# Performance work log

Hardware: AMD Instinct MI355X
Metric: run time of the kernel (lower is better)

Reference implementation:

```python
import jax, jax.numpy as jnp
import numpy as np

P = 15          # processor layers
D = 128         # node/edge feature dim (== hidden dim)
N_NODES = 10000
N_EDGES = 160000


def _mlp(x, w0, b0, w1, b1, w2, b2):
    h = jax.nn.relu(x @ w0 + b0)
    h = jax.nn.relu(h @ w1 + b1)
    return h @ w2 + b2


def setup_inputs() -> dict:
    key = jax.random.key(0)
    ks = jax.random.split(key, 20)
    inp = {
        "node_features": jax.random.normal(ks[0], (N_NODES, D), jnp.float32),
        "edge_features": jax.random.normal(ks[1], (N_EDGES, D), jnp.float32),
        "src": jax.random.randint(ks[2], (N_EDGES,), 0, N_NODES, jnp.int32),
        "dst": jax.random.randint(ks[3], (N_EDGES,), 0, N_NODES, jnp.int32),
    }
    s = 0.05
    # edge MLP: input 2*D + D = 384 -> 128 -> 128 -> 128, stacked over P layers
    inp["ew0"] = jax.random.normal(ks[4], (P, 3 * D, D), jnp.float32) * s
    inp["eb0"] = jnp.zeros((P, D), jnp.float32)
    inp["ew1"] = jax.random.normal(ks[5], (P, D, D), jnp.float32) * s
    inp["eb1"] = jnp.zeros((P, D), jnp.float32)
    inp["ew2"] = jax.random.normal(ks[6], (P, D, D), jnp.float32) * s
    inp["eb2"] = jnp.zeros((P, D), jnp.float32)
    # node MLP: input D + D = 256 -> 128 -> 128 -> 128
    inp["nw0"] = jax.random.normal(ks[7], (P, 2 * D, D), jnp.float32) * s
    inp["nb0"] = jnp.zeros((P, D), jnp.float32)
    inp["nw1"] = jax.random.normal(ks[8], (P, D, D), jnp.float32) * s
    inp["nb1"] = jnp.zeros((P, D), jnp.float32)
    inp["nw2"] = jax.random.normal(ks[9], (P, D, D), jnp.float32) * s
    inp["nb2"] = jnp.zeros((P, D), jnp.float32)
    return inp


def reference(node_features, edge_features, src, dst,
              ew0, eb0, ew1, eb1, ew2, eb2,
              nw0, nb0, nw1, nb1, nw2, nb2):
    n, e = node_features, edge_features
    for i in range(P):
        # --- edge block: gather src/dst node feats, edge MLP, residual ---
        cat_e = jnp.concatenate([n[src], n[dst], e], axis=-1)  # [E, 3D]
        e = _mlp(cat_e, ew0[i], eb0[i], ew1[i], eb1[i], ew2[i], eb2[i]) + e
        # --- node block: scatter-sum edges to dst nodes, node MLP, residual ---
        agg = jax.ops.segment_sum(e, dst, num_segments=N_NODES)  # [N, D]
        cat_n = jnp.concatenate([n, agg], axis=-1)               # [N, 2D]
        n = _mlp(cat_n, nw0[i], nb0[i], nw1[i], nb1[i], nw2[i], nb2[i]) + n
    return n
```

## Files before the change

kernel.cpp:

```cpp
#include <hip/hip_runtime.h>

#define DD 128
#define PP 15
#define NNODES 10000
#define NEDGES 160000

typedef __attribute__((ext_vector_type(8))) short bf16x8;
typedef __attribute__((ext_vector_type(4))) float f32x4;

__device__ inline ushort f2bf(float f) {
  unsigned u = __builtin_bit_cast(unsigned, f);
  u += 0x7FFFu + ((u >> 16) & 1u);
  return (ushort)(u >> 16);
}

__device__ inline float bf2f(ushort h) {
  unsigned u = ((unsigned)h) << 16;
  return __builtin_bit_cast(float, u);
}

__device__ inline f32x4 mfma16(bf16x8 a, bf16x8 b, f32x4 c) {
  return __builtin_amdgcn_mfma_f32_16x16x32_bf16(a, b, c, 0, 0, 0);
}

__global__ __launch_bounds__(256) void pack_w(const float* __restrict__ w,
                                              ushort* __restrict__ out,
                                              int K, int total) {
  int i = blockIdx.x * 256 + threadIdx.x;
  if (i >= total) return;
  int per = K * 128;
  int p = i / per, j = i % per;
  int e = j & 7;
  int lane = (j >> 3) & 63;
  int t = j >> 9;
  int nkt = K >> 5;
  int kt = t % nkt, cb = t / nkt;
  int k = kt * 32 + ((lane >> 4) << 3) + e;
  int n = (cb << 4) + (lane & 15);
  out[i] = f2bf(w[(size_t)p * per + (size_t)k * 128 + n]);
}

__global__ __launch_bounds__(256) void cvt_bf(const float* __restrict__ in,
                                              ushort* __restrict__ out, int n4) {
  int i = blockIdx.x * 256 + threadIdx.x;
  if (i >= n4) return;
  float4 v = ((const float4*)in)[i];
  ushort4 h;
  h.x = f2bf(v.x); h.y = f2bf(v.y); h.z = f2bf(v.z); h.w = f2bf(v.w);
  ((ushort4*)out)[i] = h;
}

__global__ __launch_bounds__(256) void cvt_init(const float* __restrict__ in,
                                                float* __restrict__ out_f,
                                                ushort* __restrict__ out_bf, int n4) {
  int i = blockIdx.x * 256 + threadIdx.x;
  if (i >= n4) return;
  float4 v = ((const float4*)in)[i];
  ((float4*)out_f)[i] = v;
  ushort4 h;
  h.x = f2bf(v.x); h.y = f2bf(v.y); h.z = f2bf(v.z); h.w = f2bf(v.w);
  ((ushort4*)out_bf)[i] = h;
}

__global__ __launch_bounds__(256) void hist_kernel(const int* __restrict__ dst,
                                                   int* __restrict__ cnt) {
  int i = blockIdx.x * 256 + threadIdx.x;
  if (i < NEDGES) atomicAdd(&cnt[dst[i]], 1);
}

__global__ __launch_bounds__(256) void scan_kernel(const int* __restrict__ cnt,
                                                   int* __restrict__ row_start,
                                                   int* __restrict__ cursor) {
  __shared__ int part[256];
  const int CH = (NNODES + 255) / 256;
  int t = threadIdx.x;
  int beg = t * CH, end = min(beg + CH, NNODES);
  int s = 0;
  for (int i = beg; i < end; ++i) s += cnt[i];
  part[t] = s;
  __syncthreads();
  for (int off = 1; off < 256; off <<= 1) {
    int v = (t >= off) ? part[t - off] : 0;
    __syncthreads();
    part[t] += v;
    __syncthreads();
  }
  int run = part[t] - s;
  for (int i = beg; i < end; ++i) {
    row_start[i] = run;
    cursor[i] = run;
    run += cnt[i];
  }
  if (t == 255) row_start[NNODES] = NEDGES;
}

__global__ __launch_bounds__(256) void scatter_kernel(const int* __restrict__ dst,
                                                      int* __restrict__ cursor,
                                                      int* __restrict__ eidx) {
  int i = blockIdx.x * 256 + threadIdx.x;
  if (i < NEDGES) {
    int pos = atomicAdd(&cursor[dst[i]], 1);
    eidx[pos] = i;
  }
}

__global__ __launch_bounds__(256) void agg_kernel(const ushort* __restrict__ ebf,
                                                  ushort* __restrict__ abf,
                                                  const int* __restrict__ row_start,
                                                  const int* __restrict__ eidx) {
  int wv = threadIdx.x >> 6, lane = threadIdx.x & 63;
  int node = blockIdx.x * 4 + wv;
  if (node >= NNODES) return;
  int jb = row_start[node], je = row_start[node + 1];
  float ax = 0.f, ay = 0.f, bx = 0.f, by = 0.f;
  float cx = 0.f, cy = 0.f, dx = 0.f, dy = 0.f;
  int j = jb;
  for (; j + 3 < je; j += 4) {
    int e0 = eidx[j], e1 = eidx[j + 1], e2 = eidx[j + 2], e3 = eidx[j + 3];
    uint u0 = *(const uint*)(ebf + (size_t)e0 * DD + lane * 2);
    uint u1 = *(const uint*)(ebf + (size_t)e1 * DD + lane * 2);
    uint u2 = *(const uint*)(ebf + (size_t)e2 * DD + lane * 2);
    uint u3 = *(const uint*)(ebf + (size_t)e3 * DD + lane * 2);
    ax += bf2f((ushort)u0); ay += __builtin_bit_cast(float, u0 & 0xFFFF0000u);
    bx += bf2f((ushort)u1); by += __builtin_bit_cast(float, u1 & 0xFFFF0000u);
    cx += bf2f((ushort)u2); cy += __builtin_bit_cast(float, u2 & 0xFFFF0000u);
    dx += bf2f((ushort)u3); dy += __builtin_bit_cast(float, u3 & 0xFFFF0000u);
  }
  for (; j < je; ++j) {
    int e0 = eidx[j];
    uint u0 = *(const uint*)(ebf + (size_t)e0 * DD + lane * 2);
    ax += bf2f((ushort)u0); ay += __builtin_bit_cast(float, u0 & 0xFFFF0000u);
  }
  float sx = (ax + bx) + (cx + dx);
  float sy = (ay + by) + (cy + dy);
  ushort2 h;
  h.x = f2bf(sx); h.y = f2bf(sy);
  *(ushort2*)&abf[(size_t)node * DD + lane * 2] = h;
}

__global__ __launch_bounds__(256) void edge_kernel(
    const ushort* __restrict__ nbf, ushort* __restrict__ ebf,
    const int* __restrict__ srcI, const int* __restrict__ dstI,
    const ushort* __restrict__ w0, const float* __restrict__ b0,
    const ushort* __restrict__ w1, const float* __restrict__ b1,
    const ushort* __restrict__ w2, const float* __restrict__ b2) {
  __shared__ ushort Alds[32 * 384];
  __shared__ ushort Hlds[32 * 128];
  const int tid = threadIdx.x;
  const int e0 = blockIdx.x * 32;
  const int lane = tid & 63, wv = tid >> 6;
  const int l15 = lane & 15, l4 = lane >> 4;

#pragma unroll
  for (int i = 0; i < 6; ++i) {
    int c = i * 256 + tid;
    int row = c / 48, f8 = c % 48;
    const ushort* sp;
    if (f8 < 16)       sp = nbf + (size_t)srcI[e0 + row] * DD + f8 * 8;
    else if (f8 < 32)  sp = nbf + (size_t)dstI[e0 + row] * DD + (f8 - 16) * 8;
    else               sp = ebf + (size_t)(e0 + row) * DD + (f8 - 32) * 8;
    bf16x8 v = *(const bf16x8*)sp;
    *(bf16x8*)&Alds[row * 384 + ((f8 ^ (row & 15)) * 8)] = v;
  }
  __syncthreads();

  const f32x4 z = {0.f, 0.f, 0.f, 0.f};
  const int cbA = wv * 2, cbB = wv * 2 + 1;
  f32x4 acc[2][2];

#pragma unroll
  for (int rb = 0; rb < 2; ++rb) { acc[rb][0] = z; acc[rb][1] = z; }
#pragma unroll
  for (int kt = 0; kt < 12; ++kt) {
    bf16x8 bA = *(const bf16x8*)(w0 + (size_t)((cbA * 12 + kt) * 64 + lane) * 8);
    bf16x8 bB = *(const bf16x8*)(w0 + (size_t)((cbB * 12 + kt) * 64 + lane) * 8);
#pragma unroll
    for (int rb = 0; rb < 2; ++rb) {
      int row = rb * 16 + l15;
      bf16x8 a = *(const bf16x8*)&Alds[row * 384 + (((kt * 4 + l4) ^ (row & 15)) * 8)];
      acc[rb][0] = mfma16(a, bA, acc[rb][0]);
      acc[rb][1] = mfma16(a, bB, acc[rb][1]);
    }
  }
  {
    float biasA = b0[cbA * 16 + l15], biasB = b0[cbB * 16 + l15];
#pragma unroll
    for (int cbi = 0; cbi < 2; ++cbi) {
      int col = (wv * 2 + cbi) * 16 + l15;
      float bias = cbi ? biasB : biasA;
#pragma unroll
      for (int rb = 0; rb < 2; ++rb)
#pragma unroll
        for (int r = 0; r < 4; ++r) {
          int row = rb * 16 + l4 * 4 + r;
          float v = fmaxf(acc[rb][cbi][r] + bias, 0.f);
          Hlds[row * 128 + (((col >> 3) ^ (row & 15)) * 8) + (col & 7)] = f2bf(v);
        }
    }
  }
  __syncthreads();

#pragma unroll
  for (int rb = 0; rb < 2; ++rb) { acc[rb][0] = z; acc[rb][1] = z; }
#pragma unroll
  for (int kt = 0; kt < 4; ++kt) {
    bf16x8 bA = *(const bf16x8*)(w1 + (size_t)((cbA * 4 + kt) * 64 + lane) * 8);
    bf16x8 bB = *(const bf16x8*)(w1 + (size_t)((cbB * 4 + kt) * 64 + lane) * 8);
#pragma unroll
    for (int rb = 0; rb < 2; ++rb) {
      int row = rb * 16 + l15;
      bf16x8 a = *(const bf16x8*)&Hlds[row * 128 + (((kt * 4 + l4) ^ (row & 15)) * 8)];
      acc[rb][0] = mfma16(a, bA, acc[rb][0]);
      acc[rb][1] = mfma16(a, bB, acc[rb][1]);
    }
  }
  {
    float biasA = b1[cbA * 16 + l15], biasB = b1[cbB * 16 + l15];
#pragma unroll
    for (int cbi = 0; cbi < 2; ++cbi) {
      int col = (wv * 2 + cbi) * 16 + l15;
      float bias = cbi ? biasB : biasA;
#pragma unroll
      for (int rb = 0; rb < 2; ++rb)
#pragma unroll
        for (int r = 0; r < 4; ++r) {
          int row = rb * 16 + l4 * 4 + r;
          float v = fmaxf(acc[rb][cbi][r] + bias, 0.f);
          Alds[row * 384 + (((col >> 3) ^ (row & 15)) * 8) + (col & 7)] = f2bf(v);
        }
    }
  }
  __syncthreads();

#pragma unroll
  for (int rb = 0; rb < 2; ++rb) { acc[rb][0] = z; acc[rb][1] = z; }
#pragma unroll
  for (int kt = 0; kt < 4; ++kt) {
    bf16x8 bA = *(const bf16x8*)(w2 + (size_t)((cbA * 4 + kt) * 64 + lane) * 8);
    bf16x8 bB = *(const bf16x8*)(w2 + (size_t)((cbB * 4 + kt) * 64 + lane) * 8);
#pragma unroll
    for (int rb = 0; rb < 2; ++rb) {
      int row = rb * 16 + l15;
      bf16x8 a = *(const bf16x8*)&Alds[row * 384 + (((kt * 4 + l4) ^ (row & 15)) * 8)];
      acc[rb][0] = mfma16(a, bA, acc[rb][0]);
      acc[rb][1] = mfma16(a, bB, acc[rb][1]);
    }
  }
  {
#pragma unroll
    for (int cbi = 0; cbi < 2; ++cbi) {
      int col = (wv * 2 + cbi) * 16 + l15;
      float bias = b2[col];
#pragma unroll
      for (int rb = 0; rb < 2; ++rb)
#pragma unroll
        for (int r = 0; r < 4; ++r) {
          int row = rb * 16 + l4 * 4 + r;
          float ein = bf2f(Alds[row * 384 + ((32 + ((col >> 3) ^ (row & 15))) * 8) + (col & 7)]);
          float res = ein + acc[rb][cbi][r] + bias;
          Hlds[row * 128 + (((col >> 3) ^ (row & 15)) * 8) + (col & 7)] = f2bf(res);
        }
    }
  }
  __syncthreads();
#pragma unroll
  for (int i = 0; i < 2; ++i) {
    int c = i * 256 + tid;
    int row = c >> 4, f8 = c & 15;
    bf16x8 v = *(const bf16x8*)&Hlds[row * 128 + ((f8 ^ (row & 15)) * 8)];
    *(bf16x8*)&ebf[(size_t)(e0 + row) * DD + f8 * 8] = v;
  }
}

__global__ __launch_bounds__(256) void node_kernel(
    float* __restrict__ nbuf, ushort* __restrict__ nbf,
    const ushort* __restrict__ abf,
    const ushort* __restrict__ w0, const float* __restrict__ b0,
    const ushort* __restrict__ w1, const float* __restrict__ b1,
    const ushort* __restrict__ w2, const float* __restrict__ b2) {
  __shared__ ushort Alds[32 * 256];
  __shared__ ushort Hlds[32 * 128];
  const int tid = threadIdx.x;
  const int n0 = blockIdx.x * 32;
  const int lane = tid & 63, wv = tid >> 6;
  const int l15 = lane & 15, l4 = lane >> 4;

#pragma unroll
  for (int i = 0; i < 4; ++i) {
    int c = i * 256 + tid;
    int row = c >> 5, f8 = c & 31;
    int node = n0 + row;
    bf16x8 v = {0, 0, 0, 0, 0, 0, 0, 0};
    if (node < NNODES) {
      const ushort* sp = (f8 < 16) ? nbf + (size_t)node * DD + f8 * 8
                                   : abf + (size_t)node * DD + (f8 - 16) * 8;
      v = *(const bf16x8*)sp;
    }
    *(bf16x8*)&Alds[row * 256 + ((f8 ^ (row & 15)) * 8)] = v;
  }
  __syncthreads();

  const f32x4 z = {0.f, 0.f, 0.f, 0.f};
  const int cbA = wv * 2, cbB = wv * 2 + 1;
  f32x4 acc[2][2];

#pragma unroll
  for (int rb = 0; rb < 2; ++rb) { acc[rb][0] = z; acc[rb][1] = z; }
#pragma unroll
  for (int kt = 0; kt < 8; ++kt) {
    bf16x8 bA = *(const bf16x8*)(w0 + (size_t)((cbA * 8 + kt) * 64 + lane) * 8);
    bf16x8 bB = *(const bf16x8*)(w0 + (size_t)((cbB * 8 + kt) * 64 + lane) * 8);
#pragma unroll
    for (int rb = 0; rb < 2; ++rb) {
      int row = rb * 16 + l15;
      bf16x8 a = *(const bf16x8*)&Alds[row * 256 + (((kt * 4 + l4) ^ (row & 15)) * 8)];
      acc[rb][0] = mfma16(a, bA, acc[rb][0]);
      acc[rb][1] = mfma16(a, bB, acc[rb][1]);
    }
  }
  {
    float biasA = b0[cbA * 16 + l15], biasB = b0[cbB * 16 + l15];
#pragma unroll
    for (int cbi = 0; cbi < 2; ++cbi) {
      int col = (wv * 2 + cbi) * 16 + l15;
      float bias = cbi ? biasB : biasA;
#pragma unroll
      for (int rb = 0; rb < 2; ++rb)
#pragma unroll
        for (int r = 0; r < 4; ++r) {
          int row = rb * 16 + l4 * 4 + r;
          float v = fmaxf(acc[rb][cbi][r] + bias, 0.f);
          Hlds[row * 128 + (((col >> 3) ^ (row & 15)) * 8) + (col & 7)] = f2bf(v);
        }
    }
  }
  __syncthreads();

#pragma unroll
  for (int rb = 0; rb < 2; ++rb) { acc[rb][0] = z; acc[rb][1] = z; }
#pragma unroll
  for (int kt = 0; kt < 4; ++kt) {
    bf16x8 bA = *(const bf16x8*)(w1 + (size_t)((cbA * 4 + kt) * 64 + lane) * 8);
    bf16x8 bB = *(const bf16x8*)(w1 + (size_t)((cbB * 4 + kt) * 64 + lane) * 8);
#pragma unroll
    for (int rb = 0; rb < 2; ++rb) {
      int row = rb * 16 + l15;
      bf16x8 a = *(const bf16x8*)&Hlds[row * 128 + (((kt * 4 + l4) ^ (row & 15)) * 8)];
      acc[rb][0] = mfma16(a, bA, acc[rb][0]);
      acc[rb][1] = mfma16(a, bB, acc[rb][1]);
    }
  }
  {
    float biasA = b1[cbA * 16 + l15], biasB = b1[cbB * 16 + l15];
#pragma unroll
    for (int cbi = 0; cbi < 2; ++cbi) {
      int col = (wv * 2 + cbi) * 16 + l15;
      float bias = cbi ? biasB : biasA;
#pragma unroll
      for (int rb = 0; rb < 2; ++rb)
#pragma unroll
        for (int r = 0; r < 4; ++r) {
          int row = rb * 16 + l4 * 4 + r;
          float v = fmaxf(acc[rb][cbi][r] + bias, 0.f);
          Alds[row * 256 + ((16 + ((col >> 3) ^ (row & 15))) * 8) + (col & 7)] = f2bf(v);
        }
    }
  }
  __syncthreads();

#pragma unroll
  for (int rb = 0; rb < 2; ++rb) { acc[rb][0] = z; acc[rb][1] = z; }
#pragma unroll
  for (int kt = 0; kt < 4; ++kt) {
    bf16x8 bA = *(const bf16x8*)(w2 + (size_t)((cbA * 4 + kt) * 64 + lane) * 8);
    bf16x8 bB = *(const bf16x8*)(w2 + (size_t)((cbB * 4 + kt) * 64 + lane) * 8);
#pragma unroll
    for (int rb = 0; rb < 2; ++rb) {
      int row = rb * 16 + l15;
      bf16x8 a = *(const bf16x8*)&Alds[row * 256 + ((16 + ((kt * 4 + l4) ^ (row & 15))) * 8)];
      acc[rb][0] = mfma16(a, bA, acc[rb][0]);
      acc[rb][1] = mfma16(a, bB, acc[rb][1]);
    }
  }
  {
#pragma unroll
    for (int cbi = 0; cbi < 2; ++cbi) {
      int col = (wv * 2 + cbi) * 16 + l15;
      float bias = b2[col];
#pragma unroll
      for (int rb = 0; rb < 2; ++rb)
#pragma unroll
        for (int r = 0; r < 4; ++r) {
          int row = rb * 16 + l4 * 4 + r;
          int node = n0 + row;
          if (node < NNODES) {
            size_t off = (size_t)node * DD + col;
            float res = nbuf[off] + acc[rb][cbi][r] + bias;
            nbuf[off] = res;
            nbf[off] = f2bf(res);
          }
        }
    }
  }
}

extern "C" void kernel_launch(void* const* d_in, const int* in_sizes, int n_in,
                              void* d_out, int out_size, void* d_ws, size_t ws_size,
                              hipStream_t stream) {
  const float* node_f = (const float*)d_in[0];
  const float* edge_f = (const float*)d_in[1];
  const int* srcI = (const int*)d_in[2];
  const int* dstI = (const int*)d_in[3];
  const float* ew0 = (const float*)d_in[4];
  const float* eb0 = (const float*)d_in[5];
  const float* ew1 = (const float*)d_in[6];
  const float* eb1 = (const float*)d_in[7];
  const float* ew2 = (const float*)d_in[8];
  const float* eb2 = (const float*)d_in[9];
  const float* nw0 = (const float*)d_in[10];
  const float* nb0 = (const float*)d_in[11];
  const float* nw1 = (const float*)d_in[12];
  const float* nb1 = (const float*)d_in[13];
  const float* nw2 = (const float*)d_in[14];
  const float* nb2 = (const float*)d_in[15];

  char* ws = (char*)d_ws;
  const size_t NB  = (size_t)NNODES * DD * 4;
  const size_t EBH = (size_t)NEDGES * DD * 2;
  const size_t NBH = (size_t)NNODES * DD * 2;
  ushort* ebf  = (ushort*)ws;
  float*  nbuf = (float*)(ws + EBH);
  ushort* nbf  = (ushort*)(ws + EBH + NB);
  ushort* abf  = (ushort*)(ws + EBH + NB + NBH);
  ushort* pw   = (ushort*)(ws + EBH + NB + 2 * NBH);
  ushort* pew0 = pw;
  ushort* pew1 = pew0 + 737280;
  ushort* pew2 = pew1 + 245760;
  ushort* pnw0 = pew2 + 245760;
  ushort* pnw1 = pnw0 + 491520;
  ushort* pnw2 = pnw1 + 245760;
  const size_t WBYTES = 2211840ull * 2;
  int* eidx      = (int*)(ws + EBH + NB + 2 * NBH + WBYTES);
  int* cnt       = eidx + NEDGES;
  int* row_start = cnt + NNODES;
  int* cursor    = row_start + NNODES + 1;

  {
    struct { const float* s; ushort* d; int K; } packs[6] = {
      {ew0, pew0, 384}, {ew1, pew1, 128}, {ew2, pew2, 128},
      {nw0, pnw0, 256}, {nw1, pnw1, 128}, {nw2, pnw2, 128},
    };
    for (int i = 0; i < 6; ++i) {
      int total = PP * packs[i].K * 128;
      pack_w<<<(total + 255) / 256, 256, 0, stream>>>(packs[i].s, packs[i].d,
                                                      packs[i].K, total);
    }
  }

  hipMemsetAsync(cnt, 0, NNODES * sizeof(int), stream);
  hist_kernel<<<(NEDGES + 255) / 256, 256, 0, stream>>>(dstI, cnt);
  scan_kernel<<<1, 256, 0, stream>>>(cnt, row_start, cursor);
  scatter_kernel<<<(NEDGES + 255) / 256, 256, 0, stream>>>(dstI, cursor, eidx);

  {
    int en4 = NEDGES * DD / 4, nn4 = NNODES * DD / 4;
    cvt_bf<<<(en4 + 255) / 256, 256, 0, stream>>>(edge_f, ebf, en4);
    cvt_init<<<(nn4 + 255) / 256, 256, 0, stream>>>(node_f, nbuf, nbf, nn4);
  }

  const int eblocks = NEDGES / 32;
  const int nblocks = (NNODES + 31) / 32;
  const int ablocks = (NNODES + 3) / 4;

  for (int p = 0; p < PP; ++p) {
    edge_kernel<<<eblocks, 256, 0, stream>>>(
        nbf, ebf, srcI, dstI,
        pew0 + (size_t)p * 49152, eb0 + (size_t)p * DD,
        pew1 + (size_t)p * 16384, eb1 + (size_t)p * DD,
        pew2 + (size_t)p * 16384, eb2 + (size_t)p * DD);
    agg_kernel<<<ablocks, 256, 0, stream>>>(ebf, abf, row_start, eidx);
    node_kernel<<<nblocks, 256, 0, stream>>>(
        nbuf, nbf, abf,
        pnw0 + (size_t)p * 32768, nb0 + (size_t)p * DD,
        pnw1 + (size_t)p * 16384, nb1 + (size_t)p * DD,
        pnw2 + (size_t)p * 16384, nb2 + (size_t)p * DD);
  }

  hipMemcpyAsync(d_out, nbuf, NB, hipMemcpyDeviceToDevice, stream);
}
```

Measured before the change: 1.565 ms.

## Load gathered node features directly into MFMA registers, shrink edge LDS, fuse setup kernels

The edge kernel no longer stages the src/dst node rows in a 384-wide LDS tile. Each lane now reads its gathered nbf rows straight from global memory as MFMA A-operands, and only the edge features go through a smaller LDS buffer. This cuts LDS footprint and store traffic, which may raise occupancy, at the cost of more scattered global reads per lane. The change also packs bf16 conversions with v_cvt_pk_bf16_f32, merges the six weight-pack launches and the two conversion launches into single kernels, and reuses the H buffer with an extra barrier.

```diff
diff --git a/kernel.cpp b/kernel.cpp
--- a/kernel.cpp
+++ b/kernel.cpp
@@ -19,20 +19,35 @@
   return __builtin_bit_cast(float, u);
 }
 
+__device__ inline uint cvt_pk(float lo, float hi) {
+  uint r;
+  asm("v_cvt_pk_bf16_f32 %0, %1, %2" : "=v"(r) : "v"(lo), "v"(hi));
+  return r;
+}
+
 __device__ inline f32x4 mfma16(bf16x8 a, bf16x8 b, f32x4 c) {
   return __builtin_amdgcn_mfma_f32_16x16x32_bf16(a, b, c, 0, 0, 0);
 }
 
-__global__ __launch_bounds__(256) void pack_w(const float* __restrict__ w,
-                                              ushort* __restrict__ out,
-                                              int K, int total) {
+__global__ __launch_bounds__(256) void pack_all(
+    const float* __restrict__ ew0, const float* __restrict__ ew1,
+    const float* __restrict__ ew2, const float* __restrict__ nw0,
+    const float* __restrict__ nw1, const float* __restrict__ nw2,
+    ushort* __restrict__ out) {
   int i = blockIdx.x * 256 + threadIdx.x;
-  if (i >= total) return;
+  if (i >= 2211840) return;
+  const float* w; int K; int j = i;
+  if (i < 737280)       { w = ew0; K = 384; }
+  else if (i < 983040)  { w = ew1; K = 128; j = i - 737280; }
+  else if (i < 1228800) { w = ew2; K = 128; j = i - 983040; }
+  else if (i < 1720320) { w = nw0; K = 256; j = i - 1228800; }
+  else if (i < 1966080) { w = nw1; K = 128; j = i - 1720320; }
+  else                  { w = nw2; K = 128; j = i - 1966080; }
   int per = K * 128;
-  int p = i / per, j = i % per;
-  int e = j & 7;
-  int lane = (j >> 3) & 63;
-  int t = j >> 9;
+  int p = j / per, q = j % per;
+  int e = q & 7;
+  int lane = (q >> 3) & 63;
+  int t = q >> 9;
   int nkt = K >> 5;
   int kt = t % nkt, cb = t / nkt;
   int k = kt * 32 + ((lane >> 4) << 3) + e;
@@ -40,26 +55,27 @@
   out[i] = f2bf(w[(size_t)p * per + (size_t)k * 128 + n]);
 }
 
-__global__ __launch_bounds__(256) void cvt_bf(const float* __restrict__ in,
-                                              ushort* __restrict__ out, int n4) {
+__global__ __launch_bounds__(256) void cvt_all(const float* __restrict__ ef,
+                                               const float* __restrict__ nf,
+                                               ushort* __restrict__ ebf,
+                                               float* __restrict__ nbuf,
+                                               ushort* __restrict__ nbf) {
+  const int en4 = NEDGES * DD / 4;
+  const int nn4 = NNODES * DD / 4;
   int i = blockIdx.x * 256 + threadIdx.x;
-  if (i >= n4) return;
-  float4 v = ((const float4*)in)[i];
-  ushort4 h;
-  h.x = f2bf(v.x); h.y = f2bf(v.y); h.z = f2bf(v.z); h.w = f2bf(v.w);
-  ((ushort4*)out)[i] = h;
-}
-
-__global__ __launch_bounds__(256) void cvt_init(const float* __restrict__ in,
-                                                float* __restrict__ out_f,
-                                                ushort* __restrict__ out_bf, int n4) {
-  int i = blockIdx.x * 256 + threadIdx.x;
-  if (i >= n4) return;
-  float4 v = ((const float4*)in)[i];
-  ((float4*)out_f)[i] = v;
-  ushort4 h;
-  h.x = f2bf(v.x); h.y = f2bf(v.y); h.z = f2bf(v.z); h.w = f2bf(v.w);
-  ((ushort4*)out_bf)[i] = h;
+  if (i < en4) {
+    float4 v = ((const float4*)ef)[i];
+    ushort4 h;
+    h.x = f2bf(v.x); h.y = f2bf(v.y); h.z = f2bf(v.z); h.w = f2bf(v.w);
+    ((ushort4*)ebf)[i] = h;
+  } else if (i < en4 + nn4) {
+    int k = i - en4;
+    float4 v = ((const float4*)nf)[k];
+    ((float4*)nbuf)[k] = v;
+    ushort4 h;
+    h.x = f2bf(v.x); h.y = f2bf(v.y); h.z = f2bf(v.z); h.w = f2bf(v.w);
+    ((ushort4*)nbf)[k] = h;
+  }
 }
 
 __global__ __launch_bounds__(256) void hist_kernel(const int* __restrict__ dst,
@@ -133,9 +149,7 @@
   }
   float sx = (ax + bx) + (cx + dx);
   float sy = (ay + by) + (cy + dy);
-  ushort2 h;
-  h.x = f2bf(sx); h.y = f2bf(sy);
-  *(ushort2*)&abf[(size_t)node * DD + lane * 2] = h;
+  *(uint*)&abf[(size_t)node * DD + lane * 2] = cvt_pk(sx, sy);
 }
 
 __global__ __launch_bounds__(256) void edge_kernel(
@@ -144,7 +158,7 @@
     const ushort* __restrict__ w0, const float* __restrict__ b0,
     const ushort* __restrict__ w1, const float* __restrict__ b1,
     const ushort* __restrict__ w2, const float* __restrict__ b2) {
-  __shared__ ushort Alds[32 * 384];
+  __shared__ ushort Elds[32 * 128];
   __shared__ ushort Hlds[32 * 128];
   const int tid = threadIdx.x;
   const int e0 = blockIdx.x * 32;
@@ -152,114 +166,158 @@
   const int l15 = lane & 15, l4 = lane >> 4;
 
 #pragma unroll
-  for (int i = 0; i < 6; ++i) {
+  for (int i = 0; i < 2; ++i) {
     int c = i * 256 + tid;
-    int row = c / 48, f8 = c % 48;
-    const ushort* sp;
-    if (f8 < 16)       sp = nbf + (size_t)srcI[e0 + row] * DD + f8 * 8;
-    else if (f8 < 32)  sp = nbf + (size_t)dstI[e0 + row] * DD + (f8 - 16) * 8;
-    else               sp = ebf + (size_t)(e0 + row) * DD + (f8 - 32) * 8;
-    bf16x8 v = *(const bf16x8*)sp;
-    *(bf16x8*)&Alds[row * 384 + ((f8 ^ (row & 15)) * 8)] = v;
-  }
+    int row = c >> 4, f8 = c & 15;
+    bf16x8 v = *(const bf16x8*)(ebf + (size_t)(e0 + row) * DD + f8 * 8);
+    *(bf16x8*)&Elds[row * 128 + ((f8 ^ (row & 15)) * 8)] = v;
+  }
+
+  const ushort* sp0 = nbf + (size_t)srcI[e0 + l15] * DD + l4 * 8;
+  const ushort* sp1 = nbf + (size_t)srcI[e0 + 16 + l15] * DD + l4 * 8;
+  const ushort* dp0 = nbf + (size_t)dstI[e0 + l15] * DD + l4 * 8;
+  const ushort* dp1 = nbf + (size_t)dstI[e0 + 16 + l15] * DD + l4 * 8;
   __syncthreads();
 
   const f32x4 z = {0.f, 0.f, 0.f, 0.f};
   const int cbA = wv * 2, cbB = wv * 2 + 1;
   f32x4 acc[2][2];
-
-#pragma unroll
-  for (int rb = 0; rb < 2; ++rb) { acc[rb][0] = z; acc[rb][1] = z; }
-#pragma unroll
-  for (int kt = 0; kt < 12; ++kt) {
+  acc[0][0] = z; acc[0][1] = z; acc[1][0] = z; acc[1][1] = z;
+
+#pragma unroll
+  for (int kt = 0; kt < 4; ++kt) {
     bf16x8 bA = *(const bf16x8*)(w0 + (size_t)((cbA * 12 + kt) * 64 + lane) * 8);
     bf16x8 bB = *(const bf16x8*)(w0 + (size_t)((cbB * 12 + kt) * 64 + lane) * 8);
-#pragma unroll
-    for (int rb = 0; rb < 2; ++rb) {
-      int row = rb * 16 + l15;
-      bf16x8 a = *(const bf16x8*)&Alds[row * 384 + (((kt * 4 + l4) ^ (row & 15)) * 8)];
-      acc[rb][0] = mfma16(a, bA, acc[rb][0]);
-      acc[rb][1] = mfma16(a, bB, acc[rb][1]);
-    }
-  }
+    bf16x8 a0 = *(const bf16x8*)(sp0 + kt * 32);
+    bf16x8 a1 = *(const bf16x8*)(sp1 + kt * 32);
+    acc[0][0] = mfma16(a0, bA, acc[0][0]); acc[0][1] = mfma16(a0, bB, acc[0][1]);
+    acc[1][0] = mfma16(a1, bA, acc[1][0]); acc[1][1] = mfma16(a1, bB, acc[1][1]);
+  }
+#pragma unroll
+  for (int kt = 0; kt < 4; ++kt) {
+    bf16x8 bA = *(const bf16x8*)(w0 + (size_t)((cbA * 12 + 4 + kt) * 64 + lane) * 8);
+    bf16x8 bB = *(const bf16x8*)(w0 + (size_t)((cbB * 12 + 4 + kt) * 64 + lane) * 8);
+    bf16x8 a0 = *(const bf16x8*)(dp0 + kt * 32);
+    bf16x8 a1 = *(const bf16x8*)(dp1 + kt * 32);
+    acc[0][0] = mfma16(a0, bA, acc[0][0]); acc[0][1] = mfma16(a0, bB, acc[0][1]);
+    acc[1][0] = mfma16(a1, bA, acc[1][0]); acc[1][1] = mfma16(a1, bB, acc[1][1]);
+  }
+#pragma unroll
+  for (int kt = 0; kt < 4; ++kt) {
+    bf16x8 bA = *(const bf16x8*)(w0 + (size_t)((cbA * 12 + 8 + kt) * 64 + lane) * 8);
+    bf16x8 bB = *(const bf16x8*)(w0 + (size_t)((cbB * 12 + 8 + kt) * 64 + lane) * 8);
+    int sl = ((kt * 4 + l4) ^ l15) * 8;
+    bf16x8 a0 = *(const bf16x8*)&Elds[l15 * 128 + sl];
+    bf16x8 a1 = *(const bf16x8*)&Elds[(16 + l15) * 128 + sl];
+    acc[0][0] = mfma16(a0, bA, acc[0][0]); acc[0][1] = mfma16(a0, bB, acc[0][1]);
+    acc[1][0] = mfma16(a1, bA, acc[1][0]); acc[1][1] = mfma16(a1, bB, acc[1][1]);
+  }
+
   {
     float biasA = b0[cbA * 16 + l15], biasB = b0[cbB * 16 + l15];
 #pragma unroll
     for (int cbi = 0; cbi < 2; ++cbi) {
       int col = (wv * 2 + cbi) * 16 + l15;
       float bias = cbi ? biasB : biasA;
-#pragma unroll
-      for (int rb = 0; rb < 2; ++rb)
-#pragma unroll
-        for (int r = 0; r < 4; ++r) {
-          int row = rb * 16 + l4 * 4 + r;
-          float v = fmaxf(acc[rb][cbi][r] + bias, 0.f);
-          Hlds[row * 128 + (((col >> 3) ^ (row & 15)) * 8) + (col & 7)] = f2bf(v);
-        }
-    }
-  }
-  __syncthreads();
-
-#pragma unroll
-  for (int rb = 0; rb < 2; ++rb) { acc[rb][0] = z; acc[rb][1] = z; }
+      int cs = col >> 3, c7 = col & 7;
+#pragma unroll
+      for (int rb = 0; rb < 2; ++rb) {
+        float v0 = fmaxf(acc[rb][cbi][0] + bias, 0.f);
+        float v1 = fmaxf(acc[rb][cbi][1] + bias, 0.f);
+        float v2 = fmaxf(acc[rb][cbi][2] + bias, 0.f);
+        float v3 = fmaxf(acc[rb][cbi][3] + bias, 0.f);
+        uint p01 = cvt_pk(v0, v1), p23 = cvt_pk(v2, v3);
+        int r0 = rb * 16 + l4 * 4;
+        Hlds[(r0 + 0) * 128 + ((cs ^ ((r0 + 0) & 15)) * 8) + c7] = (ushort)p01;
+        Hlds[(r0 + 1) * 128 + ((cs ^ ((r0 + 1) & 15)) * 8) + c7] = (ushort)(p01 >> 16);
+        Hlds[(r0 + 2) * 128 + ((cs ^ ((r0 + 2) & 15)) * 8) + c7] = (ushort)p23;
+        Hlds[(r0 + 3) * 128 + ((cs ^ ((r0 + 3) & 15)) * 8) + c7] = (ushort)(p23 >> 16);
+      }
+    }
+  }
+  __syncthreads();
+
+  acc[0][0] = z; acc[0][1] = z; acc[1][0] = z; acc[1][1] = z;
 #pragma unroll
   for (int kt = 0; kt < 4; ++kt) {
     bf16x8 bA = *(const bf16x8*)(w1 + (size_t)((cbA * 4 + kt) * 64 + lane) * 8);
     bf16x8 bB = *(const bf16x8*)(w1 + (size_t)((cbB * 4 + kt) * 64 + lane) * 8);
-#pragma unroll
-    for (int rb = 0; rb < 2; ++rb) {
-      int row = rb * 16 + l15;
-      bf16x8 a = *(const bf16x8*)&Hlds[row * 128 + (((kt * 4 + l4) ^ (row & 15)) * 8)];
-      acc[rb][0] = mfma16(a, bA, acc[rb][0]);
-      acc[rb][1] = mfma16(a, bB, acc[rb][1]);
-    }
-  }
+    int sl = ((kt * 4 + l4) ^ l15) * 8;
+    bf16x8 a0 = *(const bf16x8*)&Hlds[l15 * 128 + sl];
+    bf16x8 a1 = *(const bf16x8*)&Hlds[(16 + l15) * 128 + sl];
+    acc[0][0] = mfma16(a0, bA, acc[0][0]); acc[0][1] = mfma16(a0, bB, acc[0][1]);
+    acc[1][0] = mfma16(a1, bA, acc[1][0]); acc[1][1] = mfma16(a1, bB, acc[1][1]);
+  }
+  uint h2p[2][2][2];
   {
     float biasA = b1[cbA * 16 + l15], biasB = b1[cbB * 16 + l15];
 #pragma unroll
     for (int cbi = 0; cbi < 2; ++cbi) {
+      float bias = cbi ? biasB : biasA;
+#pragma unroll
+      for (int rb = 0; rb < 2; ++rb) {
+        float v0 = fmaxf(acc[rb][cbi][0] + bias, 0.f);
+        float v1 = fmaxf(acc[rb][cbi][1] + bias, 0.f);
+        float v2 = fmaxf(acc[rb][cbi][2] + bias, 0.f);
+        float v3 = fmaxf(acc[rb][cbi][3] + bias, 0.f);
+        h2p[rb][cbi][0] = cvt_pk(v0, v1);
+        h2p[rb][cbi][1] = cvt_pk(v2, v3);
+      }
+    }
+  }
+  __syncthreads();
+  {
+#pragma unroll
+    for (int cbi = 0; cbi < 2; ++cbi) {
       int col = (wv * 2 + cbi) * 16 + l15;
-      float bias = cbi ? biasB : biasA;
-#pragma unroll
-      for (int rb = 0; rb < 2; ++rb)
-#pragma unroll
-        for (int r = 0; r < 4; ++r) {
-          int row = rb * 16 + l4 * 4 + r;
-          float v = fmaxf(acc[rb][cbi][r] + bias, 0.f);
-          Alds[row * 384 + (((col >> 3) ^ (row & 15)) * 8) + (col & 7)] = f2bf(v);
-        }
-    }
-  }
-  __syncthreads();
-
-#pragma unroll
-  for (int rb = 0; rb < 2; ++rb) { acc[rb][0] = z; acc[rb][1] = z; }
+      int cs = col >> 3, c7 = col & 7;
+#pragma unroll
+      for (int rb = 0; rb < 2; ++rb) {
+        uint p01 = h2p[rb][cbi][0], p23 = h2p[rb][cbi][1];
+        int r0 = rb * 16 + l4 * 4;
+        Hlds[(r0 + 0) * 128 + ((cs ^ ((r0 + 0) & 15)) * 8) + c7] = (ushort)p01;
+        Hlds[(r0 + 1) * 128 + ((cs ^ ((r0 + 1) & 15)) * 8) + c7] = (ushort)(p01 >> 16);
+        Hlds[(r0 + 2) * 128 + ((cs ^ ((r0 + 2) & 15)) * 8) + c7] = (ushort)p23;
+        Hlds[(r0 + 3) * 128 + ((cs ^ ((r0 + 3) & 15)) * 8) + c7] = (ushort)(p23 >> 16);
+      }
+    }
+  }
+  __syncthreads();
+
+  acc[0][0] = z; acc[0][1] = z; acc[1][0] = z; acc[1][1] = z;
 #pragma unroll
   for (int kt = 0; kt < 4; ++kt) {
     bf16x8 bA = *(const bf16x8*)(w2 + (size_t)((cbA * 4 + kt) * 64 + lane) * 8);
     bf16x8 bB = *(const bf16x8*)(w2 + (size_t)((cbB * 4 + kt) * 64 + lane) * 8);
-#pragma unroll
-    for (int rb = 0; rb < 2; ++rb) {
-      int row = rb * 16 + l15;
-      bf16x8 a = *(const bf16x8*)&Alds[row * 384 + (((kt * 4 + l4) ^ (row & 15)) * 8)];
-      acc[rb][0] = mfma16(a, bA, acc[rb][0]);
-      acc[rb][1] = mfma16(a, bB, acc[rb][1]);
-    }
+    int sl = ((kt * 4 + l4) ^ l15) * 8;
+    bf16x8 a0 = *(const bf16x8*)&Hlds[l15 * 128 + sl];
+    bf16x8 a1 = *(const bf16x8*)&Hlds[(16 + l15) * 128 + sl];
+    acc[0][0] = mfma16(a0, bA, acc[0][0]); acc[0][1] = mfma16(a0, bB, acc[0][1]);
+    acc[1][0] = mfma16(a1, bA, acc[1][0]); acc[1][1] = mfma16(a1, bB, acc[1][1]);
   }
   {
 #pragma unroll
     for (int cbi = 0; cbi < 2; ++cbi) {
       int col = (wv * 2 + cbi) * 16 + l15;
       float bias = b2[col];
-#pragma unroll
-      for (int rb = 0; rb < 2; ++rb)
-#pragma unroll
-        for (int r = 0; r < 4; ++r) {
-          int row = rb * 16 + l4 * 4 + r;
-          float ein = bf2f(Alds[row * 384 + ((32 + ((col >> 3) ^ (row & 15))) * 8) + (col & 7)]);
-          float res = ein + acc[rb][cbi][r] + bias;
-          Hlds[row * 128 + (((col >> 3) ^ (row & 15)) * 8) + (col & 7)] = f2bf(res);
-        }
+      int cs = col >> 3, c7 = col & 7;
+#pragma unroll
+      for (int rb = 0; rb < 2; ++rb) {
+        int r0 = rb * 16 + l4 * 4;
+        int i0 = (r0 + 0) * 128 + ((cs ^ ((r0 + 0) & 15)) * 8) + c7;
+        int i1 = (r0 + 1) * 128 + ((cs ^ ((r0 + 1) & 15)) * 8) + c7;
+        int i2 = (r0 + 2) * 128 + ((cs ^ ((r0 + 2) & 15)) * 8) + c7;
+        int i3 = (r0 + 3) * 128 + ((cs ^ ((r0 + 3) & 15)) * 8) + c7;
+        float v0 = bf2f(Elds[i0]) + acc[rb][cbi][0] + bias;
+        float v1 = bf2f(Elds[i1]) + acc[rb][cbi][1] + bias;
+        float v2 = bf2f(Elds[i2]) + acc[rb][cbi][2] + bias;
+        float v3 = bf2f(Elds[i3]) + acc[rb][cbi][3] + bias;
+        uint p01 = cvt_pk(v0, v1), p23 = cvt_pk(v2, v3);
+        Elds[i0] = (ushort)p01;
+        Elds[i1] = (ushort)(p01 >> 16);
+        Elds[i2] = (ushort)p23;
+        Elds[i3] = (ushort)(p23 >> 16);
+      }
     }
   }
   __syncthreads();
@@ -267,7 +325,7 @@
   for (int i = 0; i < 2; ++i) {
     int c = i * 256 + tid;
     int row = c >> 4, f8 = c & 15;
-    bf16x8 v = *(const bf16x8*)&Hlds[row * 128 + ((f8 ^ (row & 15)) * 8)];
+    bf16x8 v = *(const bf16x8*)&Elds[row * 128 + ((f8 ^ (row & 15)) * 8)];
     *(bf16x8*)&ebf[(size_t)(e0 + row) * DD + f8 * 8] = v;
   }
 }
@@ -304,19 +362,16 @@
   const int cbA = wv * 2, cbB = wv * 2 + 1;
   f32x4 acc[2][2];
 
-#pragma unroll
-  for (int rb = 0; rb < 2; ++rb) { acc[rb][0] = z; acc[rb][1] = z; }
+  acc[0][0] = z; acc[0][1] = z; acc[1][0] = z; acc[1][1] = z;
 #pragma unroll
   for (int kt = 0; kt < 8; ++kt) {
     bf16x8 bA = *(const bf16x8*)(w0 + (size_t)((cbA * 8 + kt) * 64 + lane) * 8);
     bf16x8 bB = *(const bf16x8*)(w0 + (size_t)((cbB * 8 + kt) * 64 + lane) * 8);
-#pragma unroll
-    for (int rb = 0; rb < 2; ++rb) {
-      int row = rb * 16 + l15;
-      bf16x8 a = *(const bf16x8*)&Alds[row * 256 + (((kt * 4 + l4) ^ (row & 15)) * 8)];
-      acc[rb][0] = mfma16(a, bA, acc[rb][0]);
-      acc[rb][1] = mfma16(a, bB, acc[rb][1]);
-    }
+    int sl = ((kt * 4 + l4) ^ l15) * 8;
+    bf16x8 a0 = *(const bf16x8*)&Alds[l15 * 256 + sl];
+    bf16x8 a1 = *(const bf16x8*)&Alds[(16 + l15) * 256 + sl];
+    acc[0][0] = mfma16(a0, bA, acc[0][0]); acc[0][1] = mfma16(a0, bB, acc[0][1]);
+    acc[1][0] = mfma16(a1, bA, acc[1][0]); acc[1][1] = mfma16(a1, bB, acc[1][1]);
   }
   {
     float biasA = b0[cbA * 16 + l15], biasB = b0[cbB * 16 + l15];
@@ -324,31 +379,34 @@
     for (int cbi = 0; cbi < 2; ++cbi) {
       int col = (wv * 2 + cbi) * 16 + l15;
       float bias = cbi ? biasB : biasA;
-#pragma unroll
-      for (int rb = 0; rb < 2; ++rb)
-#pragma unroll
-        for (int r = 0; r < 4; ++r) {
-          int row = rb * 16 + l4 * 4 + r;
-          float v = fmaxf(acc[rb][cbi][r] + bias, 0.f);
-          Hlds[row * 128 + (((col >> 3) ^ (row & 15)) * 8) + (col & 7)] = f2bf(v);
-        }
-    }
-  }
-  __syncthreads();
-
-#pragma unroll
-  for (int rb = 0; rb < 2; ++rb) { acc[rb][0] = z; acc[rb][1] = z; }
+      int cs = col >> 3, c7 = col & 7;
+#pragma unroll
+      for (int rb = 0; rb < 2; ++rb) {
+        float v0 = fmaxf(acc[rb][cbi][0] + bias, 0.f);
+        float v1 = fmaxf(acc[rb][cbi][1] + bias, 0.f);
+        float v2 = fmaxf(acc[rb][cbi][2] + bias, 0.f);
+        float v3 = fmaxf(acc[rb][cbi][3] + bias, 0.f);
+        uint p01 = cvt_pk(v0, v1), p23 = cvt_pk(v2, v3);
+        int r0 = rb * 16 + l4 * 4;
+        Hlds[(r0 + 0) * 128 + ((cs ^ ((r0 + 0) & 15)) * 8) + c7] = (ushort)p01;
+        Hlds[(r0 + 1) * 128 + ((cs ^ ((r0 + 1) & 15)) * 8) + c7] = (ushort)(p01 >> 16);
+        Hlds[(r0 + 2) * 128 + ((cs ^ ((r0 + 2) & 15)) * 8) + c7] = (ushort)p23;
+        Hlds[(r0 + 3) * 128 + ((cs ^ ((r0 + 3) & 15)) * 8) + c7] = (ushort)(p23 >> 16);
+      }
+    }
+  }
+  __syncthreads();
+
+  acc[0][0] = z; acc[0][1] = z; acc[1][0] = z; acc[1][1] = z;
 #pragma unroll
   for (int kt = 0; kt < 4; ++kt) {
     bf16x8 bA = *(const bf16x8*)(w1 + (size_t)((cbA * 4 + kt) * 64 + lane) * 8);
     bf16x8 bB = *(const bf16x8*)(w1 + (size_t)((cbB * 4 + kt) * 64 + lane) * 8);
-#pragma unroll
-    for (int rb = 0; rb < 2; ++rb) {
-      int row = rb * 16 + l15;
-      bf16x8 a = *(const bf16x8*)&Hlds[row * 128 + (((kt * 4 + l4) ^ (row & 15)) * 8)];
-      acc[rb][0] = mfma16(a, bA, acc[rb][0]);
-      acc[rb][1] = mfma16(a, bB, acc[rb][1]);
-    }
+    int sl = ((kt * 4 + l4) ^ l15) * 8;
+    bf16x8 a0 = *(const bf16x8*)&Hlds[l15 * 128 + sl];
+    bf16x8 a1 = *(const bf16x8*)&Hlds[(16 + l15) * 128 + sl];
+    acc[0][0] = mfma16(a0, bA, acc[0][0]); acc[0][1] = mfma16(a0, bB, acc[0][1]);
+    acc[1][0] = mfma16(a1, bA, acc[1][0]); acc[1][1] = mfma16(a1, bB, acc[1][1]);
   }
   {
     float biasA = b1[cbA * 16 + l15], biasB = b1[cbB * 16 + l15];
@@ -356,31 +414,34 @@
     for (int cbi = 0; cbi < 2; ++cbi) {
       int col = (wv * 2 + cbi) * 16 + l15;
       float bias = cbi ? biasB : biasA;
-#pragma unroll
-      for (int rb = 0; rb < 2; ++rb)
-#pragma unroll
-        for (int r = 0; r < 4; ++r) {
-          int row = rb * 16 + l4 * 4 + r;
-          float v = fmaxf(acc[rb][cbi][r] + bias, 0.f);
-          Alds[row * 256 + ((16 + ((col >> 3) ^ (row & 15))) * 8) + (col & 7)] = f2bf(v);
-        }
-    }
-  }
-  __syncthreads();
-
-#pragma unroll
-  for (int rb = 0; rb < 2; ++rb) { acc[rb][0] = z; acc[rb][1] = z; }
+      int cs = col >> 3, c7 = col & 7;
+#pragma unroll
+      for (int rb = 0; rb < 2; ++rb) {
+        float v0 = fmaxf(acc[rb][cbi][0] + bias, 0.f);
+        float v1 = fmaxf(acc[rb][cbi][1] + bias, 0.f);
+        float v2 = fmaxf(acc[rb][cbi][2] + bias, 0.f);
+        float v3 = fmaxf(acc[rb][cbi][3] + bias, 0.f);
+        uint p01 = cvt_pk(v0, v1), p23 = cvt_pk(v2, v3);
+        int r0 = rb * 16 + l4 * 4;
+        Alds[(r0 + 0) * 256 + ((16 + (cs ^ ((r0 + 0) & 15))) * 8) + c7] = (ushort)p01;
+        Alds[(r0 + 1) * 256 + ((16 + (cs ^ ((r0 + 1) & 15))) * 8) + c7] = (ushort)(p01 >> 16);
+        Alds[(r0 + 2) * 256 + ((16 + (cs ^ ((r0 + 2) & 15))) * 8) + c7] = (ushort)p23;
+        Alds[(r0 + 3) * 256 + ((16 + (cs ^ ((r0 + 3) & 15))) * 8) + c7] = (ushort)(p23 >> 16);
+      }
+    }
+  }
+  __syncthreads();
+
+  acc[0][0] = z; acc[0][1] = z; acc[1][0] = z; acc[1][1] = z;
 #pragma unroll
   for (int kt = 0; kt < 4; ++kt) {
     bf16x8 bA = *(const bf16x8*)(w2 + (size_t)((cbA * 4 + kt) * 64 + lane) * 8);
     bf16x8 bB = *(const bf16x8*)(w2 + (size_t)((cbB * 4 + kt) * 64 + lane) * 8);
-#pragma unroll
-    for (int rb = 0; rb < 2; ++rb) {
-      int row = rb * 16 + l15;
-      bf16x8 a = *(const bf16x8*)&Alds[row * 256 + ((16 + ((kt * 4 + l4) ^ (row & 15))) * 8)];
-      acc[rb][0] = mfma16(a, bA, acc[rb][0]);
-      acc[rb][1] = mfma16(a, bB, acc[rb][1]);
-    }
+    int sl = (16 + ((kt * 4 + l4) ^ l15)) * 8;
+    bf16x8 a0 = *(const bf16x8*)&Alds[l15 * 256 + sl];
+    bf16x8 a1 = *(const bf16x8*)&Alds[(16 + l15) * 256 + sl];
+    acc[0][0] = mfma16(a0, bA, acc[0][0]); acc[0][1] = mfma16(a0, bB, acc[0][1]);
+    acc[1][0] = mfma16(a1, bA, acc[1][0]); acc[1][1] = mfma16(a1, bB, acc[1][1]);
   }
   {
 #pragma unroll
@@ -388,18 +449,29 @@
       int col = (wv * 2 + cbi) * 16 + l15;
       float bias = b2[col];
 #pragma unroll
-      for (int rb = 0; rb < 2; ++rb)
+      for (int rb = 0; rb < 2; ++rb) {
+        int r0 = rb * 16 + l4 * 4;
+        float res[4];
 #pragma unroll
         for (int r = 0; r < 4; ++r) {
-          int row = rb * 16 + l4 * 4 + r;
-          int node = n0 + row;
+          int node = n0 + r0 + r;
           if (node < NNODES) {
             size_t off = (size_t)node * DD + col;
-            float res = nbuf[off] + acc[rb][cbi][r] + bias;
-            nbuf[off] = res;
-            nbf[off] = f2bf(res);
+            res[r] = nbuf[off] + acc[rb][cbi][r] + bias;
+            nbuf[off] = res[r];
+          } else res[r] = 0.f;
+        }
+        uint p01 = cvt_pk(res[0], res[1]), p23 = cvt_pk(res[2], res[3]);
+#pragma unroll
+        for (int r = 0; r < 4; ++r) {
+          int node = n0 + r0 + r;
+          if (node < NNODES) {
+            ushort h = (r == 0) ? (ushort)p01 : (r == 1) ? (ushort)(p01 >> 16)
+                     : (r == 2) ? (ushort)p23 : (ushort)(p23 >> 16);
+            nbf[(size_t)node * DD + col] = h;
           }
         }
+      }
     }
   }
 }
@@ -445,17 +517,8 @@
   int* row_start = cnt + NNODES;
   int* cursor    = row_start + NNODES + 1;
 
-  {
-    struct { const float* s; ushort* d; int K; } packs[6] = {
-      {ew0, pew0, 384}, {ew1, pew1, 128}, {ew2, pew2, 128},
-      {nw0, pnw0, 256}, {nw1, pnw1, 128}, {nw2, pnw2, 128},
-    };
-    for (int i = 0; i < 6; ++i) {
-      int total = PP * packs[i].K * 128;
-      pack_w<<<(total + 255) / 256, 256, 0, stream>>>(packs[i].s, packs[i].d,
-                                                      packs[i].K, total);
-    }
-  }
+  pack_all<<<(2211840 + 255) / 256, 256, 0, stream>>>(ew0, ew1, ew2, nw0, nw1,
+                                                      nw2, pw);
 
   hipMemsetAsync(cnt, 0, NNODES * sizeof(int), stream);
   hist_kernel<<<(NEDGES + 255) / 256, 256, 0, stream>>>(dstI, cnt);
@@ -463,9 +526,8 @@
   scatter_kernel<<<(NEDGES + 255) / 256, 256, 0, stream>>>(dstI, cursor, eidx);
 
   {
-    int en4 = NEDGES * DD / 4, nn4 = NNODES * DD / 4;
-    cvt_bf<<<(en4 + 255) / 256, 256, 0, stream>>>(edge_f, ebf, en4);
-    cvt_init<<<(nn4 + 255) / 256, 256, 0, stream>>>(node_f, nbuf, nbf, nn4);
+    int tot = NEDGES * DD / 4 + NNODES * DD / 4;
+    cvt_all<<<(tot + 255) / 256, 256, 0, stream>>>(edge_f, node_f, ebf, nbuf, nbf);
   }
 
   const int eblocks = NEDGES / 32;
```

After: 1.590 ms. No clear change (+1.6%).
